# Optimization experiments

Hardware: AMD Instinct MI355X
Metric: run time of the kernel (lower is better)

## Reference

```python
import jax, jax.numpy as jnp
import numpy as np

B = 1_000_000
N_DIR, N_TRIAL = 2, 4
ALPHA, R_GAS, EPS = 0.3, 8.314462618, 1e-12
TAU_CLIP, LN_CLIP = 10.0, 20.0
EPS_FD, SIGMA, MARGIN = 1e-4, 0.05, 0.0
LAM_PHY, LAM_GD, LAM_TPD = 1.0, 0.1, 0.1


def renorm3(x):
    # clamp to >=0 and normalize so components sum to 1 (last axis)
    x = jnp.maximum(x, 0.0)
    return x / jnp.maximum(x.sum(-1, keepdims=True), EPS)


def nrtl_ln_gamma(x, T, g):
    # x: (B,3), T: (B,), g: (B,3,3) -> ln_gamma: (B,3)
    x = jnp.maximum(x, 0.0)
    Tc = jnp.maximum(T, 1.0)
    tau = jnp.clip(g / (R_GAS * jnp.maximum(Tc, EPS)[:, None, None]), -TAU_CLIP, TAU_CLIP)
    G = jnp.exp(-ALPHA * tau)
    denom = jnp.maximum(jnp.einsum('bj,bji->bi', x, G), EPS)          # (B,3)
    A = jnp.einsum('bj,bji->bi', x, tau * G)                          # (B,3), == num1 in torch
    term1 = A / denom
    W = x[:, None, :] * G / denom[:, None, :]                         # (B,3,3)
    inside = tau - (A / denom)[:, None, :]
    term2 = (W * inside).sum(-1)
    return jnp.clip(term1 + term2, -LN_CLIP, LN_CLIP)


def setup_inputs() -> dict:
    key = jax.random.key(0)
    k1, k2, k3, k4, k5, k6 = jax.random.split(key, 6)
    pred = jax.random.uniform(k1, (B, 6), dtype=jnp.float32, minval=0.01, maxval=1.0)
    target = jax.random.uniform(k2, (B, 6), dtype=jnp.float32, minval=0.01, maxval=1.0)
    T = 298.0 + 100.0 * jax.random.uniform(k3, (B,), dtype=jnp.float32)  # Kelvin
    g = 800.0 * jax.random.normal(k4, (B, 3, 3), dtype=jnp.float32)      # J/mol
    # simplex directions: zero-sum, unit-norm (matches _sample_simplex_directions)
    v = jax.random.normal(k5, (N_DIR, B, 3), dtype=jnp.float32)
    v = v - v.mean(-1, keepdims=True)
    dirs = v / jnp.maximum(jnp.linalg.norm(v, axis=-1, keepdims=True), 1e-12)
    noise = SIGMA * jax.random.normal(k6, (N_TRIAL, B, 3), dtype=jnp.float32)
    return {'pred': pred, 'target': target, 'T': T, 'g': g, 'dirs': dirs, 'noise': noise}


def reference(pred, target, T, g, dirs, noise):
    # supervised MSE on (E+R) compositions
    L_sup = jnp.mean((pred - target) ** 2)

    xE = renorm3(pred[:, :3])
    xR = renorm3(pred[:, 3:])
    ln_gE = nrtl_ln_gamma(xE, T, g)
    ln_gR = nrtl_ln_gamma(xR, T, g)
    # chemical potential residual r_k = ln(xE_k gE_k) - ln(xR_k gR_k)
    r = jnp.log(jnp.maximum(xE, EPS)) + ln_gE - (jnp.log(jnp.maximum(xR, EPS)) + ln_gR)
    L_phy = jnp.mean(r ** 2)

    lg = jax.vmap(lambda xx: nrtl_ln_gamma(xx, T, g))  # over trial/direction axis

    # Gibbs-Duhem finite-difference penalty along simplex directions
    x_p = renorm3(xE[None] + EPS_FD * dirs)            # (N_DIR,B,3)
    x_m = renorm3(xE[None] - EPS_FD * dirs)
    d_ln = (lg(x_p) - lg(x_m)) / (2.0 * EPS_FD)
    gd = (xE[None] * d_ln).sum(-1)                     # (N_DIR,B)
    L_gd = jnp.mean(gd * gd)

    # TPD stability penalty
    w = renorm3(xE[None] + noise)                      # (N_TRIAL,B,3)
    ln_gw = lg(w)
    tpd = (w * (jnp.log(jnp.maximum(w, EPS)) + ln_gw
                - jnp.log(jnp.maximum(xE, EPS))[None] - ln_gE[None])).sum(-1)
    L_tpd = jnp.mean(jnp.maximum(MARGIN - tpd, 0.0))

    return L_sup + LAM_PHY * L_phy + LAM_GD * L_gd + LAM_TPD * L_tpd
```

## Files before the change

### kernel.cpp

```cpp
#include <hip/hip_runtime.h>


constexpr float ALPHA    = 0.3f;
constexpr float R_GAS    = 8.314462618f;
constexpr float EPS      = 1e-12f;
constexpr float TAU_CLIP = 10.0f;
constexpr float LN_CLIP  = 20.0f;
constexpr float EPS_FD   = 1e-4f;

constexpr float LOG2E = 1.44269504088896340736f;
constexpr float LN2   = 0.69314718055994530942f;

__device__ __forceinline__ float clipf(float v, float lo, float hi) {
    return fminf(fmaxf(v, lo), hi);
}
__device__ __forceinline__ float fast_rcp(float x) { return __builtin_amdgcn_rcpf(x); }

struct Mats {
    float tau[3][3];
    float G[3][3];
    float tG[3][3];
};

__device__ __forceinline__ void ln_gamma3(const float x[3], const Mats& M, float lg[3]) {
    float ratio[3], invd[3];
#pragma unroll
    for (int i = 0; i < 3; ++i) {
        float d = x[0] * M.G[0][i] + x[1] * M.G[1][i] + x[2] * M.G[2][i];
        d = fmaxf(d, EPS);
        float A = x[0] * M.tG[0][i] + x[1] * M.tG[1][i] + x[2] * M.tG[2][i];
        float inv = fast_rcp(d);
        invd[i] = inv;
        ratio[i] = A * inv;
    }
#pragma unroll
    for (int i = 0; i < 3; ++i) {
        float s = ratio[i];
#pragma unroll
        for (int j = 0; j < 3; ++j) {
            s += x[j] * M.G[i][j] * invd[j] * (M.tau[i][j] - ratio[j]);
        }
        lg[i] = clipf(s, -LN_CLIP, LN_CLIP);
    }
}

__device__ __forceinline__ void renorm3(float x[3]) {
    x[0] = fmaxf(x[0], 0.0f);
    x[1] = fmaxf(x[1], 0.0f);
    x[2] = fmaxf(x[2], 0.0f);
    float inv = fast_rcp(fmaxf(x[0] + x[1] + x[2], EPS));
    x[0] *= inv; x[1] *= inv; x[2] *= inv;
}

__global__ __launch_bounds__(256) void nrtl_loss_kernel(
    const float* __restrict__ pred,
    const float* __restrict__ target,
    const float* __restrict__ Tarr,
    const float* __restrict__ g,
    const float* __restrict__ dirs,
    const float* __restrict__ noise,
    float* __restrict__ partials, int B)
{
    const int i = blockIdx.x * blockDim.x + threadIdx.x;
    float contrib = 0.0f;

    if (i < B) {
        const float* prow = pred   + (size_t)i * 6;
        const float* trow = target + (size_t)i * 6;
        const float* grow = g      + (size_t)i * 9;
        float2 p01 = *(const float2*)(prow);
        float2 p23 = *(const float2*)(prow + 2);
        float2 p45 = *(const float2*)(prow + 4);
        float2 t01 = *(const float2*)(trow);
        float2 t23 = *(const float2*)(trow + 2);
        float2 t45 = *(const float2*)(trow + 4);
        float Tv = Tarr[i];
        float gv[9];
#pragma unroll
        for (int k = 0; k < 9; ++k) gv[k] = grow[k];
        float dv[2][3];
#pragma unroll
        for (int d = 0; d < 2; ++d) {
            const float* drow = dirs + ((size_t)d * B + i) * 3;
#pragma unroll
            for (int k = 0; k < 3; ++k) dv[d][k] = drow[k];
        }
        float nv[4][3];
#pragma unroll
        for (int tr = 0; tr < 4; ++tr) {
            const float* nrow = noise + ((size_t)tr * B + i) * 3;
#pragma unroll
            for (int k = 0; k < 3; ++k) nv[tr][k] = nrow[k];
        }
        float sup;
        {
            float d0 = p01.x - t01.x, d1 = p01.y - t01.y;
            float d2 = p23.x - t23.x, d3 = p23.y - t23.y;
            float d4 = p45.x - t45.x, d5 = p45.y - t45.y;
            sup = d0 * d0 + d1 * d1 + d2 * d2 + d3 * d3 + d4 * d4 + d5 * d5;
        }

        float xE[3] = {p01.x, p01.y, p23.x};
        float xR[3] = {p23.y, p45.x, p45.y};
        renorm3(xE);
        renorm3(xR);

        const float Tc = fmaxf(Tv, 1.0f);
        const float invRT = fast_rcp(R_GAS * Tc);
        Mats M;
#pragma unroll
        for (int a = 0; a < 3; ++a) {
#pragma unroll
            for (int b = 0; b < 3; ++b) {
                float ta = clipf(gv[a * 3 + b] * invRT, -TAU_CLIP, TAU_CLIP);
                float Gv = __builtin_amdgcn_exp2f((-ALPHA * LOG2E) * ta);
                M.tau[a][b] = ta;
                M.G[a][b]   = Gv;
                M.tG[a][b]  = ta * Gv;
            }
        }

        float lgE[3], lgR[3];
        ln_gamma3(xE, M, lgE);
        ln_gamma3(xR, M, lgR);

        float logxE[3];
        float phy = 0.0f;
#pragma unroll
        for (int k = 0; k < 3; ++k) {
            logxE[k] = LN2 * __builtin_amdgcn_logf(fmaxf(xE[k], EPS));
            float logxR = LN2 * __builtin_amdgcn_logf(fmaxf(xR[k], EPS));
            float r = logxE[k] + lgE[k] - logxR - lgR[k];
            phy += r * r;
        }

        float gdsum = 0.0f;
#pragma unroll
        for (int d = 0; d < 2; ++d) {
            float xp[3], xm[3];
#pragma unroll
            for (int k = 0; k < 3; ++k) {
                xp[k] = xE[k] + EPS_FD * dv[d][k];
                xm[k] = xE[k] - EPS_FD * dv[d][k];
            }
            renorm3(xp);
            renorm3(xm);
            float lgp[3], lgm[3];
            ln_gamma3(xp, M, lgp);
            ln_gamma3(xm, M, lgm);
            float gd = 0.0f;
            const float inv2e = 0.5f / EPS_FD;
#pragma unroll
            for (int k = 0; k < 3; ++k) gd += xE[k] * ((lgp[k] - lgm[k]) * inv2e);
            gdsum += gd * gd;
        }

        float tpdsum = 0.0f;
#pragma unroll
        for (int tr = 0; tr < 4; ++tr) {
            float w[3];
#pragma unroll
            for (int k = 0; k < 3; ++k) w[k] = xE[k] + nv[tr][k];
            renorm3(w);
            float lgw[3];
            ln_gamma3(w, M, lgw);
            float tpd = 0.0f;
#pragma unroll
            for (int k = 0; k < 3; ++k) {
                float logw = LN2 * __builtin_amdgcn_logf(fmaxf(w[k], EPS));
                tpd += w[k] * (logw + lgw[k] - logxE[k] - lgE[k]);
            }
            tpdsum += fmaxf(-tpd, 0.0f);
        }

        const float invB = 1.0f / (float)B;
        contrib = invB * (sup * (1.0f / 6.0f)
                          + phy * (1.0f / 3.0f)
                          + 0.1f * gdsum * 0.5f
                          + 0.1f * tpdsum * 0.25f);
    }

#pragma unroll
    for (int off = 32; off > 0; off >>= 1)
        contrib += __shfl_down(contrib, off, 64);

    __shared__ float ssum[4];
    const int lane = threadIdx.x & 63;
    const int wid  = threadIdx.x >> 6;
    if (lane == 0) ssum[wid] = contrib;
    __syncthreads();
    if (threadIdx.x == 0) {
        partials[blockIdx.x] = ssum[0] + ssum[1] + ssum[2] + ssum[3];
    }
}

__global__ __launch_bounds__(256) void reduce_kernel(
    const float* __restrict__ partials, int n, float* __restrict__ out)
{
    double sacc = 0.0;
    for (int j = threadIdx.x; j < n; j += 256) sacc += (double)partials[j];
#pragma unroll
    for (int off = 32; off > 0; off >>= 1)
        sacc += __shfl_down(sacc, off, 64);
    __shared__ double ds[4];
    const int lane = threadIdx.x & 63;
    const int wid  = threadIdx.x >> 6;
    if (lane == 0) ds[wid] = sacc;
    __syncthreads();
    if (threadIdx.x == 0) out[0] = (float)(ds[0] + ds[1] + ds[2] + ds[3]);
}

extern "C" void kernel_launch(void* const* d_in, const int* in_sizes, int n_in,
                              void* d_out, int out_size, void* d_ws, size_t ws_size,
                              hipStream_t stream) {
    const float* pred   = (const float*)d_in[0];
    const float* target = (const float*)d_in[1];
    const float* Tarr   = (const float*)d_in[2];
    const float* g      = (const float*)d_in[3];
    const float* dirs   = (const float*)d_in[4];
    const float* noise  = (const float*)d_in[5];
    const int B = in_sizes[2];

    float* partials = (float*)d_ws;
    float* out      = (float*)d_out;

    const int block = 256;
    const int grid  = (B + block - 1) / block;
    nrtl_loss_kernel<<<grid, block, 0, stream>>>(pred, target, Tarr, g, dirs, noise, partials, B);
    reduce_kernel<<<1, block, 0, stream>>>(partials, grid, out);
}
```

Before: 181.5 us.

## Stage per-block inputs through LDS with coalesced float4 loads

Each block now cooperatively copies its 256 rows of pred, g, dirs and noise into shared memory using contiguous float4 loads, then each thread reads its own row from LDS. The supervised MSE is computed during the staging pass, and a scalar fallback path handles the partial tail block. This targets the strided, poorly coalesced per-thread global loads of 6-, 9- and 3-float rows. In exchange it uses about 33 KB of LDS per block, which may limit occupancy, adds a block barrier, and LDS reads at strides of 3, 6 and 9 words may cause bank conflicts.

```diff
diff --git a/kernel.cpp b/kernel.cpp
--- a/kernel.cpp
+++ b/kernel.cpp
@@ -61,58 +61,92 @@
     const float* __restrict__ noise,
     float* __restrict__ partials, int B)
 {
-    const int i = blockIdx.x * blockDim.x + threadIdx.x;
+    __shared__ __align__(16) float sh[8448];
+    float* s_pred  = sh;
+    float* s_g     = sh + 1536;
+    float* s_dirs  = sh + 3840;
+    float* s_noise = sh + 5376;
+
+    const int t  = threadIdx.x;
+    const int s0 = blockIdx.x * 256;
+    const int ns = min(256, B - s0);
+
+    const float invB  = 1.0f / (float)B;
+    const float SUP_W = invB * (1.0f / 6.0f);
+    const float PHY_W = invB * (1.0f / 3.0f);
+    const float GD_W  = invB * 0.1f * 0.5f;
+    const float TPD_W = invB * 0.1f * 0.25f;
+
     float contrib = 0.0f;
 
-    if (i < B) {
-        const float* prow = pred   + (size_t)i * 6;
-        const float* trow = target + (size_t)i * 6;
-        const float* grow = g      + (size_t)i * 9;
-        float2 p01 = *(const float2*)(prow);
-        float2 p23 = *(const float2*)(prow + 2);
-        float2 p45 = *(const float2*)(prow + 4);
-        float2 t01 = *(const float2*)(trow);
-        float2 t23 = *(const float2*)(trow + 2);
-        float2 t45 = *(const float2*)(trow + 4);
-        float Tv = Tarr[i];
-        float gv[9];
-#pragma unroll
-        for (int k = 0; k < 9; ++k) gv[k] = grow[k];
-        float dv[2][3];
-#pragma unroll
+    if (ns == 256) {
+        const float4* pg4 = (const float4*)(pred   + (size_t)s0 * 6);
+        const float4* tg4 = (const float4*)(target + (size_t)s0 * 6);
+        const float4* gg4 = (const float4*)(g      + (size_t)s0 * 9);
+        float4* sp4 = (float4*)s_pred;
+        float4* sg4 = (float4*)s_g;
+
+        {
+            float4 pa = pg4[t], ta = tg4[t];
+            sp4[t] = pa;
+            float dx = pa.x - ta.x, dy = pa.y - ta.y, dz = pa.z - ta.z, dw = pa.w - ta.w;
+            contrib += SUP_W * (dx * dx + dy * dy + dz * dz + dw * dw);
+            if (t < 128) {
+                float4 pb = pg4[256 + t], tb = tg4[256 + t];
+                sp4[256 + t] = pb;
+                float ex = pb.x - tb.x, ey = pb.y - tb.y, ez = pb.z - tb.z, ew = pb.w - tb.w;
+                contrib += SUP_W * (ex * ex + ey * ey + ez * ez + ew * ew);
+            }
+        }
+        sg4[t]       = gg4[t];
+        sg4[256 + t] = gg4[256 + t];
+        if (t < 64) sg4[512 + t] = gg4[512 + t];
+#pragma unroll
+        for (int d = 0; d < 2; ++d)
+            if (t < 192)
+                ((float4*)(s_dirs + d * 768))[t] =
+                    ((const float4*)(dirs + ((size_t)d * B + s0) * 3))[t];
+#pragma unroll
+        for (int tr = 0; tr < 4; ++tr)
+            if (t < 192)
+                ((float4*)(s_noise + tr * 768))[t] =
+                    ((const float4*)(noise + ((size_t)tr * B + s0) * 3))[t];
+    } else {
+        const float* pg = pred   + (size_t)s0 * 6;
+        const float* tg = target + (size_t)s0 * 6;
+        for (int j = t; j < ns * 6; j += 256) {
+            float pv = pg[j], tv = tg[j];
+            s_pred[j] = pv;
+            float d = pv - tv;
+            contrib += SUP_W * d * d;
+        }
+        const float* gg = g + (size_t)s0 * 9;
+        for (int j = t; j < ns * 9; j += 256) s_g[j] = gg[j];
         for (int d = 0; d < 2; ++d) {
-            const float* drow = dirs + ((size_t)d * B + i) * 3;
-#pragma unroll
-            for (int k = 0; k < 3; ++k) dv[d][k] = drow[k];
-        }
-        float nv[4][3];
-#pragma unroll
+            const float* dg = dirs + ((size_t)d * B + s0) * 3;
+            for (int j = t; j < ns * 3; j += 256) s_dirs[d * 768 + j] = dg[j];
+        }
         for (int tr = 0; tr < 4; ++tr) {
-            const float* nrow = noise + ((size_t)tr * B + i) * 3;
-#pragma unroll
-            for (int k = 0; k < 3; ++k) nv[tr][k] = nrow[k];
-        }
-        float sup;
-        {
-            float d0 = p01.x - t01.x, d1 = p01.y - t01.y;
-            float d2 = p23.x - t23.x, d3 = p23.y - t23.y;
-            float d4 = p45.x - t45.x, d5 = p45.y - t45.y;
-            sup = d0 * d0 + d1 * d1 + d2 * d2 + d3 * d3 + d4 * d4 + d5 * d5;
-        }
-
-        float xE[3] = {p01.x, p01.y, p23.x};
-        float xR[3] = {p23.y, p45.x, p45.y};
+            const float* ng = noise + ((size_t)tr * B + s0) * 3;
+            for (int j = t; j < ns * 3; j += 256) s_noise[tr * 768 + j] = ng[j];
+        }
+    }
+    __syncthreads();
+
+    if (t < ns) {
+        float xE[3] = {s_pred[t * 6],     s_pred[t * 6 + 1], s_pred[t * 6 + 2]};
+        float xR[3] = {s_pred[t * 6 + 3], s_pred[t * 6 + 4], s_pred[t * 6 + 5]};
         renorm3(xE);
         renorm3(xR);
 
-        const float Tc = fmaxf(Tv, 1.0f);
+        const float Tc = fmaxf(Tarr[s0 + t], 1.0f);
         const float invRT = fast_rcp(R_GAS * Tc);
         Mats M;
 #pragma unroll
         for (int a = 0; a < 3; ++a) {
 #pragma unroll
             for (int b = 0; b < 3; ++b) {
-                float ta = clipf(gv[a * 3 + b] * invRT, -TAU_CLIP, TAU_CLIP);
+                float ta = clipf(s_g[t * 9 + a * 3 + b] * invRT, -TAU_CLIP, TAU_CLIP);
                 float Gv = __builtin_amdgcn_exp2f((-ALPHA * LOG2E) * ta);
                 M.tau[a][b] = ta;
                 M.G[a][b]   = Gv;
@@ -133,6 +167,7 @@
             float r = logxE[k] + lgE[k] - logxR - lgR[k];
             phy += r * r;
         }
+        contrib += PHY_W * phy;
 
         float gdsum = 0.0f;
 #pragma unroll
@@ -140,8 +175,9 @@
             float xp[3], xm[3];
 #pragma unroll
             for (int k = 0; k < 3; ++k) {
-                xp[k] = xE[k] + EPS_FD * dv[d][k];
-                xm[k] = xE[k] - EPS_FD * dv[d][k];
+                float dvk = s_dirs[d * 768 + t * 3 + k];
+                xp[k] = xE[k] + EPS_FD * dvk;
+                xm[k] = xE[k] - EPS_FD * dvk;
             }
             renorm3(xp);
             renorm3(xm);
@@ -154,13 +190,14 @@
             for (int k = 0; k < 3; ++k) gd += xE[k] * ((lgp[k] - lgm[k]) * inv2e);
             gdsum += gd * gd;
         }
+        contrib += GD_W * gdsum;
 
         float tpdsum = 0.0f;
 #pragma unroll
         for (int tr = 0; tr < 4; ++tr) {
             float w[3];
 #pragma unroll
-            for (int k = 0; k < 3; ++k) w[k] = xE[k] + nv[tr][k];
+            for (int k = 0; k < 3; ++k) w[k] = xE[k] + s_noise[tr * 768 + t * 3 + k];
             renorm3(w);
             float lgw[3];
             ln_gamma3(w, M, lgw);
@@ -172,12 +209,7 @@
             }
             tpdsum += fmaxf(-tpd, 0.0f);
         }
-
-        const float invB = 1.0f / (float)B;
-        contrib = invB * (sup * (1.0f / 6.0f)
-                          + phy * (1.0f / 3.0f)
-                          + 0.1f * gdsum * 0.5f
-                          + 0.1f * tpdsum * 0.25f);
+        contrib += TPD_W * tpdsum;
     }
 
 #pragma unroll
```

New measurement: 192.9 us. 6.3% more time.
